# Optimization experiments

Measured on AMD Instinct MI355X. Metric: run time of the kernel, lower is better.

The kernel has to match this reference:

```python
import jax, jax.numpy as jnp
import numpy as np

SR = 48000
N_FFT = 2048
HOP = 960
N_MELS = 64
FMIN, FMAX = 20.0, 16000.0
N_DIR = 2304
B = 8
N_SAMPLES = 960000
EPS = 1e-8


def _hz_to_mel(hz):
    return 2595.0 * np.log10(1.0 + hz / 700.0)


def _mel_to_hz(mel):
    return 700.0 * (10.0 ** (mel / 2595.0) - 1.0)


def _build_mel_filterbank(n_fft, n_mels, sr, fmin, fmax):
    n_freqs = n_fft // 2 + 1
    fft_freqs = np.linspace(0.0, sr / 2.0, n_freqs)
    mel_points = np.linspace(_hz_to_mel(fmin), _hz_to_mel(fmax), n_mels + 2)
    hz_points = np.array([_mel_to_hz(m) for m in mel_points])
    fb = np.zeros((n_mels, n_freqs), dtype=np.float32)
    for m in range(1, n_mels + 1):
        f_low, f_ctr, f_high = hz_points[m - 1], hz_points[m], hz_points[m + 1]
        lower = (fft_freqs - f_low) / max(f_ctr - f_low, 1e-8)
        upper = (f_high - fft_freqs) / max(f_high - f_ctr, 1e-8)
        fb[m - 1, :] = np.maximum(0.0, np.minimum(lower, upper))
    return fb


def setup_inputs() -> dict:
    key = jax.random.key(0)
    k1, k2, k3, k4, k5, k6 = jax.random.split(key, 6)
    F_ = N_FFT // 2 + 1
    waveform = jax.random.normal(k1, (B, 2, N_SAMPLES), dtype=jnp.float32)
    W_real = jax.random.normal(k2, (N_DIR, F_), dtype=jnp.float32)
    W_imag = jax.random.normal(k3, (N_DIR, F_), dtype=jnp.float32)
    norm_hr_sq = jax.random.uniform(k4, (N_DIR, F_), dtype=jnp.float32)
    norm_hl_sq = jax.random.uniform(k5, (N_DIR, F_), dtype=jnp.float32)
    az_bin_idx = jax.random.randint(k6, (N_DIR,), 0, N_MELS)
    # deterministic buffers as in the torch module
    n = jnp.arange(N_FFT, dtype=jnp.float32)
    window = 0.5 - 0.5 * jnp.cos(2.0 * jnp.pi * n / N_FFT)  # torch.hann_window (periodic)
    mel_fb = jnp.asarray(_build_mel_filterbank(N_FFT, N_MELS, SR, FMIN, FMAX))
    return {"waveform": waveform, "W_real": W_real, "W_imag": W_imag,
            "norm_hr_sq": norm_hr_sq, "norm_hl_sq": norm_hl_sq,
            "az_bin_idx": az_bin_idx, "window": window, "mel_fb": mel_fb}


def _stft(x, window):
    # x: [B, N] -> complex [B, F, T]
    pad = N_FFT // 2
    xp = jnp.pad(x, ((0, 0), (pad, pad)))
    T = 1 + (xp.shape[-1] - N_FFT) // HOP
    starts = jnp.arange(T) * HOP
    frames = xp[:, starts[:, None] + jnp.arange(N_FFT)]  # [B, T, n_fft]
    spec = jnp.fft.rfft(frames * window, axis=-1)        # [B, T, F]
    return jnp.transpose(spec, (0, 2, 1))                # [B, F, T]


def reference(waveform, W_real, W_imag, norm_hr_sq, norm_hl_sq, az_bin_idx, window, mel_fb):
    x_L = waveform[:, 0, :]
    x_R = waveform[:, 1, :]
    X_L = _stft(x_L, window)  # [B, F, T] complex
    X_R = _stft(x_R, window)
    pow_L = jnp.abs(X_L) ** 2
    pow_R = jnp.abs(X_R) ** 2

    mel_L = jnp.einsum('mf,bft->bmt', mel_fb, pow_L)
    mel_R = jnp.einsum('mf,bft->bmt', mel_fb, pow_R)
    ch0 = 10.0 * jnp.log10(mel_L + EPS)
    ch1 = 10.0 * jnp.log10(mel_R + EPS)
    ch2 = 10.0 * jnp.log10(mel_L / (mel_R + EPS) + EPS)

    csd = X_L * jnp.conj(X_R)
    csd_r, csd_i = jnp.real(csd), jnp.imag(csd)
    mel_csd_r = jnp.einsum('mf,bft->bmt', mel_fb, csd_r)
    mel_csd_i = jnp.einsum('mf,bft->bmt', mel_fb, csd_i)
    mel_csd_norm = jnp.sqrt(mel_csd_r ** 2 + mel_csd_i ** 2 + EPS)
    ch3 = mel_csd_i / mel_csd_norm
    ch4 = mel_csd_r / mel_csd_norm

    # per-direction HRTF cross-correlation, then scatter into azimuth bins
    corr_un = (jnp.einsum('df,bft->bdt', W_real, csd_r)
               - jnp.einsum('df,bft->bdt', W_imag, csd_i))  # [B, N_DIR, T]
    n1 = jnp.einsum('df,bft->bdt', norm_hr_sq, pow_L)
    n2 = jnp.einsum('df,bft->bdt', norm_hl_sq, pow_R)
    corr = corr_un / jnp.sqrt(n1 * n2 + 1e-8)

    T = corr.shape[-1]
    hrtf = jnp.zeros((corr.shape[0], N_MELS, T), dtype=corr.dtype)
    hrtf = hrtf.at[:, az_bin_idx, :].add(corr)
    cnt = jnp.zeros((N_MELS,), dtype=corr.dtype).at[az_bin_idx].add(1.0)
    ch5 = hrtf / (cnt[None, :, None] + EPS)

    return jnp.stack([ch0, ch1, ch2, ch3, ch4, ch5], axis=1)  # [B, 6, 64, T]
```

## Files before the change

### kernel.cpp

```cpp
#include <hip/hip_runtime.h>
#include <math.h>

#define NFFT    2048
#define HOP     960
#define NMELS   64
#define NDIR    2304
#define BATCH   8
#define NSAMP   960000
#define NF      1025
#define TFRAMES 1001
#define TP      1024
#define SEG     1056
#define K2      2112
#define BKM     16
#define LDT     68

typedef unsigned short ushort_t;
typedef __attribute__((ext_vector_type(8))) short bf16x8;
typedef __attribute__((ext_vector_type(4))) float f32x4;

__device__ __forceinline__ ushort_t f2b(float x) {
  unsigned u = __float_as_uint(x);
  return (ushort_t)((u + 0x7FFFu + ((u >> 16) & 1u)) >> 16);
}
__device__ __forceinline__ float b2f(unsigned h) {
  return __uint_as_float(h << 16);
}

#define N_CORR ((size_t)BATCH * NDIR * TP)
#define N_HRTF ((size_t)BATCH * NMELS * TFRAMES)
#define N_MF   ((size_t)NMELS * SEG)
#define N_FC   ((size_t)BATCH * TP * K2)
#define N_P    ((size_t)BATCH * TP * SEG)
#define N_AC   ((size_t)NDIR * K2)
#define N_AH   ((size_t)NDIR * SEG)

__global__ __launch_bounds__(256) void prep_k(
    const float* __restrict__ Wr, const float* __restrict__ Wi,
    const float* __restrict__ Hr, const float* __restrict__ Hl,
    const float* __restrict__ mfb,
    ushort_t* __restrict__ ACh, ushort_t* __restrict__ ACl,
    ushort_t* __restrict__ AHrh, ushort_t* __restrict__ AHrl,
    ushort_t* __restrict__ AHlh, ushort_t* __restrict__ AHll,
    float* __restrict__ MFp)
{
  const size_t n1 = (size_t)NDIR * K2, n2 = (size_t)NDIR * SEG;
  const size_t tot = n1 + 2 * n2 + (size_t)NMELS * SEG;
  for (size_t idx = blockIdx.x * 256 + threadIdx.x; idx < tot; idx += (size_t)gridDim.x * 256) {
    if (idx < n1) {
      int d = idx / K2, k2 = idx - (size_t)d * K2;
      float w;
      if (k2 < SEG) w = (k2 < NF) ? Wr[(size_t)d * NF + k2] : 0.0f;
      else { int kk = k2 - SEG; w = (kk < NF) ? -Wi[(size_t)d * NF + kk] : 0.0f; }
      ushort_t h = f2b(w);
      ACh[idx] = h; ACl[idx] = f2b(w - b2f(h));
    } else if (idx < n1 + n2) {
      size_t i = idx - n1; int d = i / SEG, k = i - (size_t)d * SEG;
      float w = (k < NF) ? Hr[(size_t)d * NF + k] : 0.0f;
      ushort_t h = f2b(w);
      AHrh[i] = h; AHrl[i] = f2b(w - b2f(h));
    } else if (idx < n1 + 2 * n2) {
      size_t i = idx - n1 - n2; int d = i / SEG, k = i - (size_t)d * SEG;
      float w = (k < NF) ? Hl[(size_t)d * NF + k] : 0.0f;
      ushort_t h = f2b(w);
      AHlh[i] = h; AHll[i] = f2b(w - b2f(h));
    } else {
      size_t i = idx - n1 - 2 * n2; int m = i / SEG, k = i - (size_t)m * SEG;
      MFp[i] = (k < NF) ? mfb[(size_t)m * NF + k] : 0.0f;
    }
  }
}

__global__ __launch_bounds__(256) void stft_kernel(
    const float* __restrict__ wave, const float* __restrict__ window,
    ushort_t* __restrict__ PLh, ushort_t* __restrict__ PRh,
    ushort_t* __restrict__ FCh, ushort_t* __restrict__ FCl)
{
  __shared__ float b0r[NFFT], b0i[NFFT], b1r[NFFT], b1i[NFFT];
  __shared__ float twr[NFFT / 2], twi[NFFT / 2];

  const int tid = threadIdx.x;
  const int bt  = blockIdx.x;
  const int b   = bt / TFRAMES;
  const int t   = bt - b * TFRAMES;

  for (int j = tid; j < NFFT / 2; j += 256) {
    float ang = -6.283185307179586f * (float)j / (float)NFFT;
    float sv, cv; sincosf(ang, &sv, &cv);
    twr[j] = cv; twi[j] = sv;
  }
  const float* wL = wave + ((size_t)b * 2 + 0) * NSAMP;
  const float* wR = wave + ((size_t)b * 2 + 1) * NSAMP;
  for (int j = tid; j < NFFT; j += 256) {
    int s0 = t * HOP - (NFFT / 2) + j;
    float wv = window[j];
    float vr = 0.0f, vi = 0.0f;
    if (s0 >= 0 && s0 < NSAMP) { vr = wL[s0] * wv; vi = wR[s0] * wv; }
    b0r[j] = vr; b0i[j] = vi;
  }
  __syncthreads();

  float *sr = b0r, *si = b0i, *dr = b1r, *di = b1i;
  int s = 1;
  for (int stage = 0; stage < 11; ++stage) {
    #pragma unroll 4
    for (int i = tid; i < NFFT / 2; i += 256) {
      int ps = i & ~(s - 1), q = i & (s - 1);
      float wr = twr[ps], wi = twi[ps];
      float ar = sr[i], ai = si[i];
      float br = sr[i + NFFT / 2], bi = si[i + NFFT / 2];
      int d0 = (ps << 1) + q;
      dr[d0] = ar + br; di[d0] = ai + bi;
      float xr = ar - br, xi = ai - bi;
      dr[d0 + s] = xr * wr - xi * wi;
      di[d0 + s] = xr * wi + xi * wr;
    }
    __syncthreads();
    float* tp = sr; sr = dr; dr = tp;
    tp = si; si = di; di = tp;
    s <<= 1;
  }

  const size_t rb = (size_t)b * TP + t;
  for (int f = tid; f < SEG; f += 256) {
    float pl = 0.f, pr = 0.f, cr = 0.f, ci = 0.f;
    if (f < NF) {
      int fc = (NFFT - f) & (NFFT - 1);
      float ar = sr[f], ai = si[f];
      float br = sr[fc], bi = si[fc];
      float lr = 0.5f * (ar + br), li = 0.5f * (ai - bi);
      float rr = 0.5f * (ai + bi), ri = 0.5f * (br - ar);
      pl = lr * lr + li * li;
      pr = rr * rr + ri * ri;
      cr = lr * rr + li * ri;
      ci = li * rr - lr * ri;
    }
    PLh[rb * SEG + f] = f2b(pl);
    PRh[rb * SEG + f] = f2b(pr);
    ushort_t crh = f2b(cr), cih = f2b(ci);
    FCh[rb * K2 + f]       = crh;
    FCh[rb * K2 + SEG + f] = cih;
    FCl[rb * K2 + f]       = f2b(cr - b2f(crh));
    FCl[rb * K2 + SEG + f] = f2b(ci - b2f(cih));
  }
}

#define GL16(gp, loff) \
  __builtin_amdgcn_global_load_lds((const __attribute__((address_space(1))) void*)(gp), \
      (__attribute__((address_space(3))) void*)(smem + (loff)), 16, 0, 0)

__global__ __launch_bounds__(256, 2) void gemm_c(
    const ushort_t* __restrict__ Ah, const ushort_t* __restrict__ Al,
    const ushort_t* __restrict__ Bh, float* __restrict__ Cout)
{
  __shared__ __align__(16) char smem[24576];
  const int tid = threadIdx.x;
  const int wave = tid >> 6, lane = tid & 63;
  const int b  = blockIdx.z;
  const int d0 = blockIdx.y * 128;
  const int t0 = blockIdx.x * 128;
  const int wr = wave >> 1, wc = wave & 1;

  const int srow = lane >> 2;
  const int skb  = (lane & 3) * 8;
  const int c0 = wave, c1 = wave + 4;
  const size_t ar0 = (size_t)(d0 + c0 * 16 + srow) * K2 + skb;
  const size_t ar1 = (size_t)(d0 + c1 * 16 + srow) * K2 + skb;
  const size_t br0 = ((size_t)b * TP + t0 + c0 * 16 + srow) * K2 + skb;
  const size_t br1 = ((size_t)b * TP + t0 + c1 * 16 + srow) * K2 + skb;

  f32x4 acc[4][4];
  #pragma unroll
  for (int i = 0; i < 4; ++i)
    #pragma unroll
    for (int j = 0; j < 4; ++j) acc[i][j] = (f32x4){0.f, 0.f, 0.f, 0.f};

  const int frow = (lane & 15) * 64;
  const int fk   = (lane >> 4) * 16;

  for (int k0 = 0; k0 < K2; k0 += 32) {
    GL16(Ah + ar0 + k0, 0     + c0 * 1024);
    GL16(Ah + ar1 + k0, 0     + c1 * 1024);
    GL16(Al + ar0 + k0, 8192  + c0 * 1024);
    GL16(Al + ar1 + k0, 8192  + c1 * 1024);
    GL16(Bh + br0 + k0, 16384 + c0 * 1024);
    GL16(Bh + br1 + k0, 16384 + c1 * 1024);
    __syncthreads();
    bf16x8 ah[4], al[4], bh[4];
    #pragma unroll
    for (int f = 0; f < 4; ++f) {
      ah[f] = *(const bf16x8*)(smem +         wr * 4096 + f * 1024 + frow + fk);
      al[f] = *(const bf16x8*)(smem + 8192  + wr * 4096 + f * 1024 + frow + fk);
      bh[f] = *(const bf16x8*)(smem + 16384 + wc * 4096 + f * 1024 + frow + fk);
    }
    #pragma unroll
    for (int i = 0; i < 4; ++i)
      #pragma unroll
      for (int j = 0; j < 4; ++j) {
        acc[i][j] = __builtin_amdgcn_mfma_f32_16x16x32_bf16(ah[i], bh[j], acc[i][j], 0, 0, 0);
        acc[i][j] = __builtin_amdgcn_mfma_f32_16x16x32_bf16(al[i], bh[j], acc[i][j], 0, 0, 0);
      }
    __syncthreads();
  }

  const int orow = (lane >> 4) * 4, ocol = lane & 15;
  #pragma unroll
  for (int i = 0; i < 4; ++i) {
    int d = d0 + wr * 64 + i * 16 + orow;
    #pragma unroll
    for (int j = 0; j < 4; ++j) {
      int t = t0 + wc * 64 + j * 16 + ocol;
      float* p = Cout + ((size_t)b * NDIR + d) * TP + t;
      #pragma unroll
      for (int r = 0; r < 4; ++r) p[(size_t)r * TP] = acc[i][j][r];
    }
  }
}

__global__ __launch_bounds__(256, 2) void gemm_n12(
    const ushort_t* __restrict__ A1h, const ushort_t* __restrict__ A1l,
    const ushort_t* __restrict__ A2h, const ushort_t* __restrict__ A2l,
    const ushort_t* __restrict__ B1,  const ushort_t* __restrict__ B2,
    const float* __restrict__ corr_un, const int* __restrict__ az,
    float* __restrict__ hrtf)
{
  __shared__ __align__(16) char smem[49152];
  const int tid = threadIdx.x;
  const int wave = tid >> 6, lane = tid & 63;
  const int b  = blockIdx.z;
  const int d0 = blockIdx.y * 128;
  const int t0 = blockIdx.x * 128;
  const int wr = wave >> 1, wc = wave & 1;

  const int srow = lane >> 2;
  const int skb  = (lane & 3) * 8;
  const int c0 = wave, c1 = wave + 4;
  const size_t ar0 = (size_t)(d0 + c0 * 16 + srow) * SEG + skb;
  const size_t ar1 = (size_t)(d0 + c1 * 16 + srow) * SEG + skb;
  const size_t br0 = ((size_t)b * TP + t0 + c0 * 16 + srow) * SEG + skb;
  const size_t br1 = ((size_t)b * TP + t0 + c1 * 16 + srow) * SEG + skb;

  f32x4 acc1[4][4], acc2[4][4];
  #pragma unroll
  for (int i = 0; i < 4; ++i)
    #pragma unroll
    for (int j = 0; j < 4; ++j) {
      acc1[i][j] = (f32x4){0.f, 0.f, 0.f, 0.f};
      acc2[i][j] = (f32x4){0.f, 0.f, 0.f, 0.f};
    }

  const int frow = (lane & 15) * 64;
  const int fk   = (lane >> 4) * 16;

  for (int k0 = 0; k0 < SEG; k0 += 32) {
    GL16(A1h + ar0 + k0, 0     + c0 * 1024);
    GL16(A1h + ar1 + k0, 0     + c1 * 1024);
    GL16(A1l + ar0 + k0, 8192  + c0 * 1024);
    GL16(A1l + ar1 + k0, 8192  + c1 * 1024);
    GL16(A2h + ar0 + k0, 16384 + c0 * 1024);
    GL16(A2h + ar1 + k0, 16384 + c1 * 1024);
    GL16(A2l + ar0 + k0, 24576 + c0 * 1024);
    GL16(A2l + ar1 + k0, 24576 + c1 * 1024);
    GL16(B1  + br0 + k0, 32768 + c0 * 1024);
    GL16(B1  + br1 + k0, 32768 + c1 * 1024);
    GL16(B2  + br0 + k0, 40960 + c0 * 1024);
    GL16(B2  + br1 + k0, 40960 + c1 * 1024);
    __syncthreads();
    bf16x8 b1f[4], b2f_[4];
    #pragma unroll
    for (int f = 0; f < 4; ++f) {
      b1f[f]  = *(const bf16x8*)(smem + 32768 + wc * 4096 + f * 1024 + frow + fk);
      b2f_[f] = *(const bf16x8*)(smem + 40960 + wc * 4096 + f * 1024 + frow + fk);
    }
    #pragma unroll
    for (int i = 0; i < 4; ++i) {
      bf16x8 a1h = *(const bf16x8*)(smem +         wr * 4096 + i * 1024 + frow + fk);
      bf16x8 a1l = *(const bf16x8*)(smem + 8192  + wr * 4096 + i * 1024 + frow + fk);
      bf16x8 a2h = *(const bf16x8*)(smem + 16384 + wr * 4096 + i * 1024 + frow + fk);
      bf16x8 a2l = *(const bf16x8*)(smem + 24576 + wr * 4096 + i * 1024 + frow + fk);
      #pragma unroll
      for (int j = 0; j < 4; ++j) {
        acc1[i][j] = __builtin_amdgcn_mfma_f32_16x16x32_bf16(a1h, b1f[j],  acc1[i][j], 0, 0, 0);
        acc1[i][j] = __builtin_amdgcn_mfma_f32_16x16x32_bf16(a1l, b1f[j],  acc1[i][j], 0, 0, 0);
        acc2[i][j] = __builtin_amdgcn_mfma_f32_16x16x32_bf16(a2h, b2f_[j], acc2[i][j], 0, 0, 0);
        acc2[i][j] = __builtin_amdgcn_mfma_f32_16x16x32_bf16(a2l, b2f_[j], acc2[i][j], 0, 0, 0);
      }
    }
    __syncthreads();
  }

  const int orow = (lane >> 4) * 4, ocol = lane & 15;
  #pragma unroll
  for (int i = 0; i < 4; ++i) {
    int dbase = d0 + wr * 64 + i * 16 + orow;
    #pragma unroll
    for (int j = 0; j < 4; ++j) {
      int t = t0 + wc * 64 + j * 16 + ocol;
      if (t < TFRAMES) {
        #pragma unroll
        for (int r = 0; r < 4; ++r) {
          int d = dbase + r;
          float n1 = acc1[i][j][r], n2 = acc2[i][j][r];
          float cu = corr_un[((size_t)b * NDIR + d) * TP + t];
          float cval = cu / sqrtf(n1 * n2 + 1e-8f);
          unsafeAtomicAdd(hrtf + ((size_t)b * NMELS + az[d]) * TFRAMES + t, cval);
        }
      }
    }
  }
}

__global__ __launch_bounds__(256) void mel_gemm(
    const float* __restrict__ MF,
    const ushort_t* __restrict__ PLh, const ushort_t* __restrict__ PRh,
    const ushort_t* __restrict__ FCh, const ushort_t* __restrict__ FCl,
    float* __restrict__ out)
{
  __shared__ float As[BKM][LDT];
  __shared__ float Bs[4][BKM][LDT];
  const int b  = blockIdx.y;
  const int t0 = blockIdx.x * 64;
  const int tid = threadIdx.x;
  const int tx = tid & 15, ty = tid >> 4;
  const int lr = tid >> 2, lk = (tid & 3) * 4;

  float aL[4][4] = {}, aR[4][4] = {}, aC[4][4] = {}, aI[4][4] = {};

  const size_t rb = (size_t)b * TP + t0 + lr;
  const ushort_t* Bp[4] = {PLh, PRh, FCh, FCh + SEG};
  const ushort_t* Bl[4] = {PLh, PRh, FCl, FCl + SEG};
  const size_t   Bst[4] = {SEG, SEG, K2, K2};

  for (int k0 = 0; k0 < SEG; k0 += BKM) {
    {
      float4 a = *(const float4*)(MF + (size_t)lr * SEG + k0 + lk);
      As[lk + 0][lr] = a.x; As[lk + 1][lr] = a.y;
      As[lk + 2][lr] = a.z; As[lk + 3][lr] = a.w;
    }
    #pragma unroll
    for (int m = 0; m < 4; ++m) {
      uint2 v = *(const uint2*)(Bp[m] + rb * Bst[m] + k0 + lk);
      float f0 = b2f(v.x & 0xffffu), f1 = b2f(v.x >> 16);
      float f2 = b2f(v.y & 0xffffu), f3 = b2f(v.y >> 16);
      if (m >= 2) {
        uint2 w = *(const uint2*)(Bl[m] + rb * Bst[m] + k0 + lk);
        f0 += b2f(w.x & 0xffffu); f1 += b2f(w.x >> 16);
        f2 += b2f(w.y & 0xffffu); f3 += b2f(w.y >> 16);
      }
      Bs[m][lk + 0][lr] = f0; Bs[m][lk + 1][lr] = f1;
      Bs[m][lk + 2][lr] = f2; Bs[m][lk + 3][lr] = f3;
    }
    __syncthreads();
    #pragma unroll
    for (int kk = 0; kk < BKM; ++kk) {
      float4 mf4 = *(const float4*)&As[kk][ty << 2];
      float4 pl4 = *(const float4*)&Bs[0][kk][tx << 2];
      float4 pr4 = *(const float4*)&Bs[1][kk][tx << 2];
      float4 cr4 = *(const float4*)&Bs[2][kk][tx << 2];
      float4 ci4 = *(const float4*)&Bs[3][kk][tx << 2];
      const float* mf = (const float*)&mf4;
      const float* pl = (const float*)&pl4; const float* pr = (const float*)&pr4;
      const float* cr = (const float*)&cr4; const float* ci = (const float*)&ci4;
      #pragma unroll
      for (int i = 0; i < 4; ++i)
        #pragma unroll
        for (int j = 0; j < 4; ++j) {
          aL[i][j] = fmaf(mf[i], pl[j], aL[i][j]);
          aR[i][j] = fmaf(mf[i], pr[j], aR[i][j]);
          aC[i][j] = fmaf(mf[i], cr[j], aC[i][j]);
          aI[i][j] = fmaf(mf[i], ci[j], aI[i][j]);
        }
    }
    __syncthreads();
  }

  #pragma unroll
  for (int i = 0; i < 4; ++i) {
    int m = (ty << 2) + i;
    #pragma unroll
    for (int j = 0; j < 4; ++j) {
      int t = t0 + (tx << 2) + j;
      if (t < TFRAMES) {
        float mlv = aL[i][j], mrv = aR[i][j], crv = aC[i][j], civ = aI[i][j];
        float ch0 = 10.0f * log10f(mlv + 1e-8f);
        float ch1 = 10.0f * log10f(mrv + 1e-8f);
        float ch2 = 10.0f * log10f(mlv / (mrv + 1e-8f) + 1e-8f);
        float nrm = sqrtf(crv * crv + civ * civ + 1e-8f);
        float ch3 = civ / nrm;
        float ch4 = crv / nrm;
        size_t bb = (size_t)b * 6 * NMELS;
        out[(bb + 0 * NMELS + m) * TFRAMES + t] = ch0;
        out[(bb + 1 * NMELS + m) * TFRAMES + t] = ch1;
        out[(bb + 2 * NMELS + m) * TFRAMES + t] = ch2;
        out[(bb + 3 * NMELS + m) * TFRAMES + t] = ch3;
        out[(bb + 4 * NMELS + m) * TFRAMES + t] = ch4;
      }
    }
  }
}

__global__ __launch_bounds__(256) void finalize_k(
    const float* __restrict__ hrtf, const int* __restrict__ az,
    float* __restrict__ out)
{
  __shared__ int red[256];
  const int m = blockIdx.x, b = blockIdx.y, tid = threadIdx.x;
  int c = 0;
  for (int j = tid; j < NDIR; j += 256) c += (az[j] == m) ? 1 : 0;
  red[tid] = c;
  __syncthreads();
  for (int st = 128; st > 0; st >>= 1) {
    if (tid < st) red[tid] += red[tid + st];
    __syncthreads();
  }
  float inv = 1.0f / ((float)red[0] + 1e-8f);
  const float* src = hrtf + ((size_t)b * NMELS + m) * TFRAMES;
  float* dst = out + (((size_t)b * 6 + 5) * NMELS + m) * TFRAMES;
  for (int t = tid; t < TFRAMES; t += 256) dst[t] = src[t] * inv;
}

extern "C" void kernel_launch(void* const* d_in, const int* in_sizes, int n_in,
                              void* d_out, int out_size, void* d_ws, size_t ws_size,
                              hipStream_t stream) {
  const float* wave   = (const float*)d_in[0];
  const float* W_real = (const float*)d_in[1];
  const float* W_imag = (const float*)d_in[2];
  const float* Nhr    = (const float*)d_in[3];
  const float* Nhl    = (const float*)d_in[4];
  const int*   az     = (const int*)  d_in[5];
  const float* window = (const float*)d_in[6];
  const float* mel_fb = (const float*)d_in[7];
  float* out = (float*)d_out;

  float* fw = (float*)d_ws;
  float* corr_un = fw;
  float* hrtf    = corr_un + N_CORR;
  float* MFp     = hrtf + N_HRTF;
  ushort_t* ub   = (ushort_t*)(MFp + N_MF);
  ushort_t* FCh  = ub;
  ushort_t* FCl  = FCh + N_FC;
  ushort_t* PLh  = FCl + N_FC;
  ushort_t* PRh  = PLh + N_P;
  ushort_t* ACh  = PRh + N_P;
  ushort_t* ACl  = ACh + N_AC;
  ushort_t* AHrh = ACl + N_AC;
  ushort_t* AHrl = AHrh + N_AH;
  ushort_t* AHlh = AHrl + N_AH;
  ushort_t* AHll = AHlh + N_AH;

  hipMemsetAsync(hrtf, 0, sizeof(float) * N_HRTF, stream);

  prep_k<<<2048, 256, 0, stream>>>(W_real, W_imag, Nhr, Nhl, mel_fb,
                                   ACh, ACl, AHrh, AHrl, AHlh, AHll, MFp);

  stft_kernel<<<BATCH * TFRAMES, 256, 0, stream>>>(wave, window, PLh, PRh, FCh, FCl);

  gemm_c<<<dim3(8, 18, BATCH), 256, 0, stream>>>(ACh, ACl, FCh, corr_un);

  gemm_n12<<<dim3(8, 18, BATCH), 256, 0, stream>>>(AHrh, AHrl, AHlh, AHll,
                                                   PLh, PRh, corr_un, az, hrtf);

  mel_gemm<<<dim3(16, BATCH), 256, 0, stream>>>(MFp, PLh, PRh, FCh, FCl, out);

  finalize_k<<<dim3(NMELS, BATCH), 256, 0, stream>>>(hrtf, az, out);
}
```

Measured before the change: 908.1 us.

## Drop split-bf16 weights, split norm GEMMs, store intermediates in bf16 with XCD-aware tiling

The weight matrices are now kept only as a single bf16 copy instead of a hi/lo pair, which halves the MFMA count and the A-operand loads in the correlation and norm GEMMs. The fused dual-norm GEMM is split into two kernels. The corr_un and n1 intermediates are stored as bf16, and a 1D grid is remapped so neighbouring tiles land on the same XCD, with occupancy raised to 3 blocks per CU. The cost is lower precision in the weights and intermediates, plus an extra kernel launch and an extra round trip for n1.

```diff
diff --git a/kernel.cpp b/kernel.cpp
--- a/kernel.cpp
+++ b/kernel.cpp
@@ -14,6 +14,7 @@
 #define K2      2112
 #define BKM     16
 #define LDT     68
+#define NWG     1152
 
 typedef unsigned short ushort_t;
 typedef __attribute__((ext_vector_type(8))) short bf16x8;
@@ -27,9 +28,9 @@
   return __uint_as_float(h << 16);
 }
 
-#define N_CORR ((size_t)BATCH * NDIR * TP)
 #define N_HRTF ((size_t)BATCH * NMELS * TFRAMES)
 #define N_MF   ((size_t)NMELS * SEG)
+#define N_CORR ((size_t)BATCH * NDIR * TP)
 #define N_FC   ((size_t)BATCH * TP * K2)
 #define N_P    ((size_t)BATCH * TP * SEG)
 #define N_AC   ((size_t)NDIR * K2)
@@ -39,10 +40,8 @@
     const float* __restrict__ Wr, const float* __restrict__ Wi,
     const float* __restrict__ Hr, const float* __restrict__ Hl,
     const float* __restrict__ mfb,
-    ushort_t* __restrict__ ACh, ushort_t* __restrict__ ACl,
-    ushort_t* __restrict__ AHrh, ushort_t* __restrict__ AHrl,
-    ushort_t* __restrict__ AHlh, ushort_t* __restrict__ AHll,
-    float* __restrict__ MFp)
+    ushort_t* __restrict__ ACh, ushort_t* __restrict__ AHrh,
+    ushort_t* __restrict__ AHlh, float* __restrict__ MFp)
 {
   const size_t n1 = (size_t)NDIR * K2, n2 = (size_t)NDIR * SEG;
   const size_t tot = n1 + 2 * n2 + (size_t)NMELS * SEG;
@@ -52,18 +51,13 @@
       float w;
       if (k2 < SEG) w = (k2 < NF) ? Wr[(size_t)d * NF + k2] : 0.0f;
       else { int kk = k2 - SEG; w = (kk < NF) ? -Wi[(size_t)d * NF + kk] : 0.0f; }
-      ushort_t h = f2b(w);
-      ACh[idx] = h; ACl[idx] = f2b(w - b2f(h));
+      ACh[idx] = f2b(w);
     } else if (idx < n1 + n2) {
       size_t i = idx - n1; int d = i / SEG, k = i - (size_t)d * SEG;
-      float w = (k < NF) ? Hr[(size_t)d * NF + k] : 0.0f;
-      ushort_t h = f2b(w);
-      AHrh[i] = h; AHrl[i] = f2b(w - b2f(h));
+      AHrh[i] = f2b((k < NF) ? Hr[(size_t)d * NF + k] : 0.0f);
     } else if (idx < n1 + 2 * n2) {
       size_t i = idx - n1 - n2; int d = i / SEG, k = i - (size_t)d * SEG;
-      float w = (k < NF) ? Hl[(size_t)d * NF + k] : 0.0f;
-      ushort_t h = f2b(w);
-      AHlh[i] = h; AHll[i] = f2b(w - b2f(h));
+      AHlh[i] = f2b((k < NF) ? Hl[(size_t)d * NF + k] : 0.0f);
     } else {
       size_t i = idx - n1 - 2 * n2; int m = i / SEG, k = i - (size_t)m * SEG;
       MFp[i] = (k < NF) ? mfb[(size_t)m * NF + k] : 0.0f;
@@ -149,20 +143,23 @@
   __builtin_amdgcn_global_load_lds((const __attribute__((address_space(1))) void*)(gp), \
       (__attribute__((address_space(3))) void*)(smem + (loff)), 16, 0, 0)
 
-__global__ __launch_bounds__(256, 2) void gemm_c(
-    const ushort_t* __restrict__ Ah, const ushort_t* __restrict__ Al,
-    const ushort_t* __restrict__ Bh, float* __restrict__ Cout)
-{
-  __shared__ __align__(16) char smem[24576];
+#define XCD_DECODE() \
+  int logical = (blockIdx.x & 7) * (NWG / 8) + (blockIdx.x >> 3); \
+  int dt = logical % 18; int rq = logical / 18;                   \
+  int tt = rq & 7; int b = rq >> 3;                               \
+  const int d0 = dt * 128; const int t0 = tt * 128;
+
+__global__ __launch_bounds__(256, 3) void gemm_c(
+    const ushort_t* __restrict__ A, const ushort_t* __restrict__ B,
+    ushort_t* __restrict__ Cout)
+{
+  __shared__ __align__(16) char smem[16384];
   const int tid = threadIdx.x;
   const int wave = tid >> 6, lane = tid & 63;
-  const int b  = blockIdx.z;
-  const int d0 = blockIdx.y * 128;
-  const int t0 = blockIdx.x * 128;
+  XCD_DECODE();
   const int wr = wave >> 1, wc = wave & 1;
 
-  const int srow = lane >> 2;
-  const int skb  = (lane & 3) * 8;
+  const int srow = lane >> 2, skb = (lane & 3) * 8;
   const int c0 = wave, c1 = wave + 4;
   const size_t ar0 = (size_t)(d0 + c0 * 16 + srow) * K2 + skb;
   const size_t ar1 = (size_t)(d0 + c1 * 16 + srow) * K2 + skb;
@@ -175,31 +172,25 @@
     #pragma unroll
     for (int j = 0; j < 4; ++j) acc[i][j] = (f32x4){0.f, 0.f, 0.f, 0.f};
 
-  const int frow = (lane & 15) * 64;
-  const int fk   = (lane >> 4) * 16;
+  const int frow = (lane & 15) * 64, fk = (lane >> 4) * 16;
 
   for (int k0 = 0; k0 < K2; k0 += 32) {
-    GL16(Ah + ar0 + k0, 0     + c0 * 1024);
-    GL16(Ah + ar1 + k0, 0     + c1 * 1024);
-    GL16(Al + ar0 + k0, 8192  + c0 * 1024);
-    GL16(Al + ar1 + k0, 8192  + c1 * 1024);
-    GL16(Bh + br0 + k0, 16384 + c0 * 1024);
-    GL16(Bh + br1 + k0, 16384 + c1 * 1024);
-    __syncthreads();
-    bf16x8 ah[4], al[4], bh[4];
+    GL16(A + ar0 + k0, 0    + c0 * 1024);
+    GL16(A + ar1 + k0, 0    + c1 * 1024);
+    GL16(B + br0 + k0, 8192 + c0 * 1024);
+    GL16(B + br1 + k0, 8192 + c1 * 1024);
+    __syncthreads();
+    bf16x8 af[4], bf[4];
     #pragma unroll
     for (int f = 0; f < 4; ++f) {
-      ah[f] = *(const bf16x8*)(smem +         wr * 4096 + f * 1024 + frow + fk);
-      al[f] = *(const bf16x8*)(smem + 8192  + wr * 4096 + f * 1024 + frow + fk);
-      bh[f] = *(const bf16x8*)(smem + 16384 + wc * 4096 + f * 1024 + frow + fk);
+      af[f] = *(const bf16x8*)(smem +        wr * 4096 + f * 1024 + frow + fk);
+      bf[f] = *(const bf16x8*)(smem + 8192 + wc * 4096 + f * 1024 + frow + fk);
     }
     #pragma unroll
     for (int i = 0; i < 4; ++i)
       #pragma unroll
-      for (int j = 0; j < 4; ++j) {
-        acc[i][j] = __builtin_amdgcn_mfma_f32_16x16x32_bf16(ah[i], bh[j], acc[i][j], 0, 0, 0);
-        acc[i][j] = __builtin_amdgcn_mfma_f32_16x16x32_bf16(al[i], bh[j], acc[i][j], 0, 0, 0);
-      }
+      for (int j = 0; j < 4; ++j)
+        acc[i][j] = __builtin_amdgcn_mfma_f32_16x16x32_bf16(af[i], bf[j], acc[i][j], 0, 0, 0);
     __syncthreads();
   }
 
@@ -210,82 +201,115 @@
     #pragma unroll
     for (int j = 0; j < 4; ++j) {
       int t = t0 + wc * 64 + j * 16 + ocol;
-      float* p = Cout + ((size_t)b * NDIR + d) * TP + t;
-      #pragma unroll
-      for (int r = 0; r < 4; ++r) p[(size_t)r * TP] = acc[i][j][r];
-    }
-  }
-}
-
-__global__ __launch_bounds__(256, 2) void gemm_n12(
-    const ushort_t* __restrict__ A1h, const ushort_t* __restrict__ A1l,
-    const ushort_t* __restrict__ A2h, const ushort_t* __restrict__ A2l,
-    const ushort_t* __restrict__ B1,  const ushort_t* __restrict__ B2,
-    const float* __restrict__ corr_un, const int* __restrict__ az,
-    float* __restrict__ hrtf)
-{
-  __shared__ __align__(16) char smem[49152];
+      ushort_t* p = Cout + ((size_t)b * NDIR + d) * TP + t;
+      #pragma unroll
+      for (int r = 0; r < 4; ++r) p[(size_t)r * TP] = f2b(acc[i][j][r]);
+    }
+  }
+}
+
+__global__ __launch_bounds__(256, 3) void gemm_n1(
+    const ushort_t* __restrict__ A, const ushort_t* __restrict__ B,
+    ushort_t* __restrict__ N1)
+{
+  __shared__ __align__(16) char smem[16384];
   const int tid = threadIdx.x;
   const int wave = tid >> 6, lane = tid & 63;
-  const int b  = blockIdx.z;
-  const int d0 = blockIdx.y * 128;
-  const int t0 = blockIdx.x * 128;
+  XCD_DECODE();
   const int wr = wave >> 1, wc = wave & 1;
 
-  const int srow = lane >> 2;
-  const int skb  = (lane & 3) * 8;
+  const int srow = lane >> 2, skb = (lane & 3) * 8;
   const int c0 = wave, c1 = wave + 4;
   const size_t ar0 = (size_t)(d0 + c0 * 16 + srow) * SEG + skb;
   const size_t ar1 = (size_t)(d0 + c1 * 16 + srow) * SEG + skb;
   const size_t br0 = ((size_t)b * TP + t0 + c0 * 16 + srow) * SEG + skb;
   const size_t br1 = ((size_t)b * TP + t0 + c1 * 16 + srow) * SEG + skb;
 
-  f32x4 acc1[4][4], acc2[4][4];
+  f32x4 acc[4][4];
   #pragma unroll
   for (int i = 0; i < 4; ++i)
     #pragma unroll
+    for (int j = 0; j < 4; ++j) acc[i][j] = (f32x4){0.f, 0.f, 0.f, 0.f};
+
+  const int frow = (lane & 15) * 64, fk = (lane >> 4) * 16;
+
+  for (int k0 = 0; k0 < SEG; k0 += 32) {
+    GL16(A + ar0 + k0, 0    + c0 * 1024);
+    GL16(A + ar1 + k0, 0    + c1 * 1024);
+    GL16(B + br0 + k0, 8192 + c0 * 1024);
+    GL16(B + br1 + k0, 8192 + c1 * 1024);
+    __syncthreads();
+    bf16x8 af[4], bf[4];
+    #pragma unroll
+    for (int f = 0; f < 4; ++f) {
+      af[f] = *(const bf16x8*)(smem +        wr * 4096 + f * 1024 + frow + fk);
+      bf[f] = *(const bf16x8*)(smem + 8192 + wc * 4096 + f * 1024 + frow + fk);
+    }
+    #pragma unroll
+    for (int i = 0; i < 4; ++i)
+      #pragma unroll
+      for (int j = 0; j < 4; ++j)
+        acc[i][j] = __builtin_amdgcn_mfma_f32_16x16x32_bf16(af[i], bf[j], acc[i][j], 0, 0, 0);
+    __syncthreads();
+  }
+
+  const int orow = (lane >> 4) * 4, ocol = lane & 15;
+  #pragma unroll
+  for (int i = 0; i < 4; ++i) {
+    int d = d0 + wr * 64 + i * 16 + orow;
+    #pragma unroll
     for (int j = 0; j < 4; ++j) {
-      acc1[i][j] = (f32x4){0.f, 0.f, 0.f, 0.f};
-      acc2[i][j] = (f32x4){0.f, 0.f, 0.f, 0.f};
-    }
-
-  const int frow = (lane & 15) * 64;
-  const int fk   = (lane >> 4) * 16;
+      int t = t0 + wc * 64 + j * 16 + ocol;
+      ushort_t* p = N1 + ((size_t)b * NDIR + d) * TP + t;
+      #pragma unroll
+      for (int r = 0; r < 4; ++r) p[(size_t)r * TP] = f2b(acc[i][j][r]);
+    }
+  }
+}
+
+__global__ __launch_bounds__(256, 3) void gemm_n2(
+    const ushort_t* __restrict__ A, const ushort_t* __restrict__ B,
+    const ushort_t* __restrict__ CU, const ushort_t* __restrict__ N1,
+    const int* __restrict__ az, float* __restrict__ hrtf)
+{
+  __shared__ __align__(16) char smem[16384];
+  const int tid = threadIdx.x;
+  const int wave = tid >> 6, lane = tid & 63;
+  XCD_DECODE();
+  const int wr = wave >> 1, wc = wave & 1;
+
+  const int srow = lane >> 2, skb = (lane & 3) * 8;
+  const int c0 = wave, c1 = wave + 4;
+  const size_t ar0 = (size_t)(d0 + c0 * 16 + srow) * SEG + skb;
+  const size_t ar1 = (size_t)(d0 + c1 * 16 + srow) * SEG + skb;
+  const size_t br0 = ((size_t)b * TP + t0 + c0 * 16 + srow) * SEG + skb;
+  const size_t br1 = ((size_t)b * TP + t0 + c1 * 16 + srow) * SEG + skb;
+
+  f32x4 acc[4][4];
+  #pragma unroll
+  for (int i = 0; i < 4; ++i)
+    #pragma unroll
+    for (int j = 0; j < 4; ++j) acc[i][j] = (f32x4){0.f, 0.f, 0.f, 0.f};
+
+  const int frow = (lane & 15) * 64, fk = (lane >> 4) * 16;
 
   for (int k0 = 0; k0 < SEG; k0 += 32) {
-    GL16(A1h + ar0 + k0, 0     + c0 * 1024);
-    GL16(A1h + ar1 + k0, 0     + c1 * 1024);
-    GL16(A1l + ar0 + k0, 8192  + c0 * 1024);
-    GL16(A1l + ar1 + k0, 8192  + c1 * 1024);
-    GL16(A2h + ar0 + k0, 16384 + c0 * 1024);
-    GL16(A2h + ar1 + k0, 16384 + c1 * 1024);
-    GL16(A2l + ar0 + k0, 24576 + c0 * 1024);
-    GL16(A2l + ar1 + k0, 24576 + c1 * 1024);
-    GL16(B1  + br0 + k0, 32768 + c0 * 1024);
-    GL16(B1  + br1 + k0, 32768 + c1 * 1024);
-    GL16(B2  + br0 + k0, 40960 + c0 * 1024);
-    GL16(B2  + br1 + k0, 40960 + c1 * 1024);
-    __syncthreads();
-    bf16x8 b1f[4], b2f_[4];
+    GL16(A + ar0 + k0, 0    + c0 * 1024);
+    GL16(A + ar1 + k0, 0    + c1 * 1024);
+    GL16(B + br0 + k0, 8192 + c0 * 1024);
+    GL16(B + br1 + k0, 8192 + c1 * 1024);
+    __syncthreads();
+    bf16x8 af[4], bf[4];
     #pragma unroll
     for (int f = 0; f < 4; ++f) {
-      b1f[f]  = *(const bf16x8*)(smem + 32768 + wc * 4096 + f * 1024 + frow + fk);
-      b2f_[f] = *(const bf16x8*)(smem + 40960 + wc * 4096 + f * 1024 + frow + fk);
-    }
-    #pragma unroll
-    for (int i = 0; i < 4; ++i) {
-      bf16x8 a1h = *(const bf16x8*)(smem +         wr * 4096 + i * 1024 + frow + fk);
-      bf16x8 a1l = *(const bf16x8*)(smem + 8192  + wr * 4096 + i * 1024 + frow + fk);
-      bf16x8 a2h = *(const bf16x8*)(smem + 16384 + wr * 4096 + i * 1024 + frow + fk);
-      bf16x8 a2l = *(const bf16x8*)(smem + 24576 + wr * 4096 + i * 1024 + frow + fk);
-      #pragma unroll
-      for (int j = 0; j < 4; ++j) {
-        acc1[i][j] = __builtin_amdgcn_mfma_f32_16x16x32_bf16(a1h, b1f[j],  acc1[i][j], 0, 0, 0);
-        acc1[i][j] = __builtin_amdgcn_mfma_f32_16x16x32_bf16(a1l, b1f[j],  acc1[i][j], 0, 0, 0);
-        acc2[i][j] = __builtin_amdgcn_mfma_f32_16x16x32_bf16(a2h, b2f_[j], acc2[i][j], 0, 0, 0);
-        acc2[i][j] = __builtin_amdgcn_mfma_f32_16x16x32_bf16(a2l, b2f_[j], acc2[i][j], 0, 0, 0);
-      }
-    }
+      af[f] = *(const bf16x8*)(smem +        wr * 4096 + f * 1024 + frow + fk);
+      bf[f] = *(const bf16x8*)(smem + 8192 + wc * 4096 + f * 1024 + frow + fk);
+    }
+    #pragma unroll
+    for (int i = 0; i < 4; ++i)
+      #pragma unroll
+      for (int j = 0; j < 4; ++j)
+        acc[i][j] = __builtin_amdgcn_mfma_f32_16x16x32_bf16(af[i], bf[j], acc[i][j], 0, 0, 0);
     __syncthreads();
   }
 
@@ -300,9 +324,11 @@
         #pragma unroll
         for (int r = 0; r < 4; ++r) {
           int d = dbase + r;
-          float n1 = acc1[i][j][r], n2 = acc2[i][j][r];
-          float cu = corr_un[((size_t)b * NDIR + d) * TP + t];
-          float cval = cu / sqrtf(n1 * n2 + 1e-8f);
+          size_t off = ((size_t)b * NDIR + d) * TP + t;
+          float n1v = b2f(N1[off]);
+          float n2v = acc[i][j][r];
+          float cu  = b2f(CU[off]);
+          float cval = cu / sqrtf(n1v * n2v + 1e-8f);
           unsafeAtomicAdd(hrtf + ((size_t)b * NMELS + az[d]) * TFRAMES + t, cval);
         }
       }
@@ -432,33 +458,30 @@
   const float* mel_fb = (const float*)d_in[7];
   float* out = (float*)d_out;
 
-  float* fw = (float*)d_ws;
-  float* corr_un = fw;
-  float* hrtf    = corr_un + N_CORR;
+  float* fw      = (float*)d_ws;
+  float* hrtf    = fw;
   float* MFp     = hrtf + N_HRTF;
   ushort_t* ub   = (ushort_t*)(MFp + N_MF);
-  ushort_t* FCh  = ub;
+  ushort_t* corr = ub;
+  ushort_t* n1b  = corr + N_CORR;
+  ushort_t* FCh  = n1b + N_CORR;
   ushort_t* FCl  = FCh + N_FC;
   ushort_t* PLh  = FCl + N_FC;
   ushort_t* PRh  = PLh + N_P;
   ushort_t* ACh  = PRh + N_P;
-  ushort_t* ACl  = ACh + N_AC;
-  ushort_t* AHrh = ACl + N_AC;
-  ushort_t* AHrl = AHrh + N_AH;
-  ushort_t* AHlh = AHrl + N_AH;
-  ushort_t* AHll = AHlh + N_AH;
+  ushort_t* AHrh = ACh + N_AC;
+  ushort_t* AHlh = AHrh + N_AH;
 
   hipMemsetAsync(hrtf, 0, sizeof(float) * N_HRTF, stream);
 
   prep_k<<<2048, 256, 0, stream>>>(W_real, W_imag, Nhr, Nhl, mel_fb,
-                                   ACh, ACl, AHrh, AHrl, AHlh, AHll, MFp);
+                                   ACh, AHrh, AHlh, MFp);
 
   stft_kernel<<<BATCH * TFRAMES, 256, 0, stream>>>(wave, window, PLh, PRh, FCh, FCl);
 
-  gemm_c<<<dim3(8, 18, BATCH), 256, 0, stream>>>(ACh, ACl, FCh, corr_un);
-
-  gemm_n12<<<dim3(8, 18, BATCH), 256, 0, stream>>>(AHrh, AHrl, AHlh, AHll,
-                                                   PLh, PRh, corr_un, az, hrtf);
+  gemm_c <<<NWG, 256, 0, stream>>>(ACh, FCh, corr);
+  gemm_n1<<<NWG, 256, 0, stream>>>(AHrh, PLh, n1b);
+  gemm_n2<<<NWG, 256, 0, stream>>>(AHlh, PRh, corr, n1b, az, hrtf);
 
   mel_gemm<<<dim3(16, BATCH), 256, 0, stream>>>(MFp, PLh, PRh, FCh, FCl, out);
 
```

New measurement: 757.4 us. -16.6%, faster.
